# Optimization experiments

Hardware: AMD Instinct MI355X
Metric: run time of the kernel (lower is better)

## Reference

```python
import jax, jax.numpy as jnp
import numpy as np

FEATURE_SIZE = 100000
FIELD_SIZE = 39
EMBED_SIZE = 16
BATCH = 4096


def setup_inputs() -> dict:
    key = jax.random.key(0)
    k1, k2, k3, k4 = jax.random.split(key, 4)
    feature_idx = jax.random.randint(k1, (BATCH, FIELD_SIZE), 0, FEATURE_SIZE)
    feature_values = jax.random.uniform(k2, (BATCH, FIELD_SIZE), dtype=jnp.float32)
    feature_embeddings = jax.random.normal(
        k3, (FEATURE_SIZE, FIELD_SIZE, EMBED_SIZE), dtype=jnp.float32)
    weights_first_order = jax.random.normal(k4, (FEATURE_SIZE, 1), dtype=jnp.float32)
    fm_bias = jnp.zeros((1,), dtype=jnp.float32)
    return {
        "feature_idx": feature_idx,
        "feature_values": feature_values,
        "feature_embeddings": feature_embeddings,
        "weights_first_order": weights_first_order,
        "fm_bias": fm_bias,
    }


def reference(feature_idx, feature_values, feature_embeddings, weights_first_order, fm_bias):
    # First order: gather per-feature scalar weights -> [B, F]
    w1 = weights_first_order[feature_idx, 0]
    first_order = jnp.sum(feature_values * w1, axis=1, keepdims=True)  # [B,1]

    # Field-aware gather: E[b, i, f, :] = feature_embeddings[idx[b,i], f, :]
    E = feature_embeddings[feature_idx]  # [B, F, F, E]

    # S[b,i,j] = <v_{i,fj}, v_{j,fi}>  (dot over embedding dim)
    S = jnp.einsum('bije,bjie->bij', E, E)  # [B, F, F]

    vv = feature_values[:, :, None] * feature_values[:, None, :]  # [B, F, F]
    F = feature_idx.shape[1]
    upper = jnp.triu(jnp.ones((F, F), dtype=bool), k=1)  # i < j pairs
    second_order = jnp.sum(jnp.where(upper, S * vv, 0.0), axis=(1, 2))[:, None]  # [B,1]

    return second_order + first_order + fm_bias
```

## Files before the change

### kernel.cpp

```cpp
#include <hip/hip_runtime.h>
#include <hip/hip_fp16.h>

#define BATCH 4096
#define FIELD 39
#define EMBED 16
#define ROW_F4 (FIELD * EMBED / 4)
#define TOT_F4 (FIELD * ROW_F4)
#define NPAIRS (FIELD * (FIELD - 1))
#define NTASK2 (NPAIRS * 2)
#define BLOCK 1024
#define NWAVES (BLOCK / 64)
#define SITER ((TOT_F4 + BLOCK - 1) / BLOCK)
#define CITER ((NTASK2 + BLOCK - 1) / BLOCK)

__global__ __launch_bounds__(BLOCK, 8) void ffm_kernel(
    const int*   __restrict__ idx,
    const float* __restrict__ vals,
    const float* __restrict__ emb,
    const float* __restrict__ w1,
    const float* __restrict__ bias,
    float*       __restrict__ out)
{
    const int b   = blockIdx.x;
    const int tid = threadIdx.x;

    __shared__ __align__(16) __half s_emb[FIELD * FIELD * EMBED];
    __shared__ int    s_idx[FIELD];
    __shared__ float  s_val[FIELD];
    __shared__ float  s_red[NWAVES];

    if (tid < FIELD) {
        s_idx[tid] = idx[b * FIELD + tid];
        s_val[tid] = vals[b * FIELD + tid];
    }
    __syncthreads();

    const float4* emb4 = (const float4*)emb;
    float4 g[SITER];
    #pragma unroll
    for (int it = 0; it < SITER; ++it) {
        int t  = tid + it * BLOCK;
        int tc = t < TOT_F4 ? t : TOT_F4 - 1;
        int i  = tc / ROW_F4;
        int off = tc - i * ROW_F4;
        g[it] = emb4[s_idx[i] * ROW_F4 + off];
    }

    float acc = 0.0f;
    if (tid < FIELD) {
        acc = s_val[tid] * w1[s_idx[tid]];
    }

    __half2* s2 = (__half2*)s_emb;
    #pragma unroll
    for (int it = 0; it < SITER; ++it) {
        int t = tid + it * BLOCK;
        if (t < TOT_F4) {
            s2[t * 2]     = __floats2half2_rn(g[it].x, g[it].y);
            s2[t * 2 + 1] = __floats2half2_rn(g[it].z, g[it].w);
        }
    }
    __syncthreads();

    #pragma unroll
    for (int it = 0; it < CITER; ++it) {
        int t = tid + it * BLOCK;
        if (t < NTASK2) {
            int p = t >> 1;
            int h = t & 1;
            int i = p / (FIELD - 1);
            int r = p - i * (FIELD - 1);
            int j = r + (r >= i ? 1 : 0);
            float4 av = *(const float4*)&s_emb[(i * FIELD + j) * EMBED + h * 8];
            float4 cv = *(const float4*)&s_emb[(j * FIELD + i) * EMBED + h * 8];
            const __half2* ah = (const __half2*)&av;
            const __half2* ch = (const __half2*)&cv;
            float dot = 0.0f;
            #pragma unroll
            for (int k = 0; k < 4; ++k) {
                float2 a = __half22float2(ah[k]);
                float2 c = __half22float2(ch[k]);
                dot += a.x * c.x + a.y * c.y;
            }
            acc += dot * (0.5f * s_val[i] * s_val[j]);
        }
    }

    #pragma unroll
    for (int off = 32; off > 0; off >>= 1)
        acc += __shfl_down(acc, off, 64);

    const int wave = tid >> 6;
    const int lane = tid & 63;
    if (lane == 0) s_red[wave] = acc;
    __syncthreads();

    if (tid == 0) {
        float s = 0.0f;
        #pragma unroll
        for (int w = 0; w < NWAVES; ++w) s += s_red[w];
        out[b] = s + bias[0];
    }
}

extern "C" void kernel_launch(void* const* d_in, const int* in_sizes, int n_in,
                              void* d_out, int out_size, void* d_ws, size_t ws_size,
                              hipStream_t stream) {
    const int*   idx  = (const int*)d_in[0];
    const float* vals = (const float*)d_in[1];
    const float* emb  = (const float*)d_in[2];
    const float* w1   = (const float*)d_in[3];
    const float* bias = (const float*)d_in[4];
    float* out = (float*)d_out;

    ffm_kernel<<<BATCH, BLOCK, 0, stream>>>(idx, vals, emb, w1, bias, out);
}
```

Before: 344.6 us.

## Process multiple batch rows per block with prefetch of next row's embeddings

Switches from one block per batch row to a persistent grid of 512 blocks that each process 8 rows. While the current row's pairwise dot products run from shared memory, the next row's embedding gather is issued into registers, overlapping global loads with compute. Gather addresses are precomputed and packed once per block. In exchange there is less block-level parallelism, and holding the prefetched registers may raise register pressure.

```diff
diff --git a/kernel.cpp b/kernel.cpp
--- a/kernel.cpp
+++ b/kernel.cpp
@@ -2,16 +2,18 @@
 #include <hip/hip_fp16.h>
 
 #define BATCH 4096
-#define FIELD 39
-#define EMBED 16
-#define ROW_F4 (FIELD * EMBED / 4)
-#define TOT_F4 (FIELD * ROW_F4)
-#define NPAIRS (FIELD * (FIELD - 1))
+#define F 39
+#define E 16
+#define ROW_F4 (F * E / 4)
+#define TOT_F4 (F * ROW_F4)
+#define NPAIRS (F * (F - 1))
 #define NTASK2 (NPAIRS * 2)
 #define BLOCK 1024
 #define NWAVES (BLOCK / 64)
-#define SITER ((TOT_F4 + BLOCK - 1) / BLOCK)
-#define CITER ((NTASK2 + BLOCK - 1) / BLOCK)
+#define GRID 512
+#define ROWS (BATCH / GRID)
+#define SITER 6
+#define CITER 3
 
 __global__ __launch_bounds__(BLOCK, 8) void ffm_kernel(
     const int*   __restrict__ idx,
@@ -21,85 +23,104 @@
     const float* __restrict__ bias,
     float*       __restrict__ out)
 {
-    const int b   = blockIdx.x;
     const int tid = threadIdx.x;
+    const int b0  = blockIdx.x * ROWS;
 
-    __shared__ __align__(16) __half s_emb[FIELD * FIELD * EMBED];
-    __shared__ int    s_idx[FIELD];
-    __shared__ float  s_val[FIELD];
-    __shared__ float  s_red[NWAVES];
+    __shared__ __align__(16) __half s_emb[F * F * E];
+    __shared__ int   s_idx[ROWS][F];
+    __shared__ float s_val[ROWS][F];
+    __shared__ float s_red[NWAVES];
 
-    if (tid < FIELD) {
-        s_idx[tid] = idx[b * FIELD + tid];
-        s_val[tid] = vals[b * FIELD + tid];
+    if (tid < ROWS * F) {
+        ((int*)s_idx)[tid]   = idx[b0 * F + tid];
+        ((float*)s_val)[tid] = vals[b0 * F + tid];
     }
     __syncthreads();
 
-    const float4* emb4 = (const float4*)emb;
-    float4 g[SITER];
+    int cpk[SITER];
     #pragma unroll
-    for (int it = 0; it < SITER; ++it) {
-        int t  = tid + it * BLOCK;
+    for (int k = 0; k < SITER; ++k) {
+        int t  = tid + k * BLOCK;
         int tc = t < TOT_F4 ? t : TOT_F4 - 1;
-        int i  = tc / ROW_F4;
-        int off = tc - i * ROW_F4;
-        g[it] = emb4[s_idx[i] * ROW_F4 + off];
+        int ci = tc / ROW_F4;
+        cpk[k] = (ci << 16) | (tc - ci * ROW_F4);
     }
 
-    float acc = 0.0f;
-    if (tid < FIELD) {
-        acc = s_val[tid] * w1[s_idx[tid]];
-    }
+    const float4* emb4 = (const float4*)emb;
+    __half2* s2 = (__half2*)s_emb;
+    float4 g[SITER];
 
-    __half2* s2 = (__half2*)s_emb;
     #pragma unroll
-    for (int it = 0; it < SITER; ++it) {
-        int t = tid + it * BLOCK;
+    for (int k = 0; k < SITER; ++k)
+        g[k] = emb4[s_idx[0][cpk[k] >> 16] * ROW_F4 + (cpk[k] & 0xffff)];
+    #pragma unroll
+    for (int k = 0; k < SITER; ++k) {
+        int t = tid + k * BLOCK;
         if (t < TOT_F4) {
-            s2[t * 2]     = __floats2half2_rn(g[it].x, g[it].y);
-            s2[t * 2 + 1] = __floats2half2_rn(g[it].z, g[it].w);
+            s2[t * 2]     = __floats2half2_rn(g[k].x, g[k].y);
+            s2[t * 2 + 1] = __floats2half2_rn(g[k].z, g[k].w);
         }
     }
     __syncthreads();
 
-    #pragma unroll
-    for (int it = 0; it < CITER; ++it) {
-        int t = tid + it * BLOCK;
-        if (t < NTASK2) {
-            int p = t >> 1;
-            int h = t & 1;
-            int i = p / (FIELD - 1);
-            int r = p - i * (FIELD - 1);
-            int j = r + (r >= i ? 1 : 0);
-            float4 av = *(const float4*)&s_emb[(i * FIELD + j) * EMBED + h * 8];
-            float4 cv = *(const float4*)&s_emb[(j * FIELD + i) * EMBED + h * 8];
-            const __half2* ah = (const __half2*)&av;
-            const __half2* ch = (const __half2*)&cv;
-            float dot = 0.0f;
+    for (int r = 0; r < ROWS; ++r) {
+        if (r + 1 < ROWS) {
             #pragma unroll
-            for (int k = 0; k < 4; ++k) {
-                float2 a = __half22float2(ah[k]);
-                float2 c = __half22float2(ch[k]);
-                dot += a.x * c.x + a.y * c.y;
+            for (int k = 0; k < SITER; ++k)
+                g[k] = emb4[s_idx[r + 1][cpk[k] >> 16] * ROW_F4 + (cpk[k] & 0xffff)];
+        }
+
+        float acc = 0.0f;
+        if (tid < F) acc = s_val[r][tid] * w1[s_idx[r][tid]];
+
+        #pragma unroll
+        for (int it = 0; it < CITER; ++it) {
+            int t = tid + it * BLOCK;
+            if (t < NTASK2) {
+                int p = t >> 1;
+                int h = t & 1;
+                int i = p / (F - 1);
+                int q = p - i * (F - 1);
+                int j = q + (q >= i ? 1 : 0);
+                float4 av = *(const float4*)&s_emb[(i * F + j) * E + h * 8];
+                float4 cv = *(const float4*)&s_emb[(j * F + i) * E + h * 8];
+                const __half2* ah = (const __half2*)&av;
+                const __half2* ch = (const __half2*)&cv;
+                float dot = 0.0f;
+                #pragma unroll
+                for (int k = 0; k < 4; ++k) {
+                    float2 a = __half22float2(ah[k]);
+                    float2 c = __half22float2(ch[k]);
+                    dot += a.x * c.x + a.y * c.y;
+                }
+                acc += dot * (0.5f * s_val[r][i] * s_val[r][j]);
             }
-            acc += dot * (0.5f * s_val[i] * s_val[j]);
         }
-    }
 
-    #pragma unroll
-    for (int off = 32; off > 0; off >>= 1)
-        acc += __shfl_down(acc, off, 64);
+        #pragma unroll
+        for (int off = 32; off > 0; off >>= 1)
+            acc += __shfl_down(acc, off, 64);
+        if ((tid & 63) == 0) s_red[tid >> 6] = acc;
+        __syncthreads();
 
-    const int wave = tid >> 6;
-    const int lane = tid & 63;
-    if (lane == 0) s_red[wave] = acc;
-    __syncthreads();
+        if (tid == 0) {
+            float s = 0.0f;
+            #pragma unroll
+            for (int w = 0; w < NWAVES; ++w) s += s_red[w];
+            out[b0 + r] = s + bias[0];
+        }
 
-    if (tid == 0) {
-        float s = 0.0f;
-        #pragma unroll
-        for (int w = 0; w < NWAVES; ++w) s += s_red[w];
-        out[b] = s + bias[0];
+        if (r + 1 < ROWS) {
+            #pragma unroll
+            for (int k = 0; k < SITER; ++k) {
+                int t = tid + k * BLOCK;
+                if (t < TOT_F4) {
+                    s2[t * 2]     = __floats2half2_rn(g[k].x, g[k].y);
+                    s2[t * 2 + 1] = __floats2half2_rn(g[k].z, g[k].w);
+                }
+            }
+            __syncthreads();
+        }
     }
 }
 
@@ -113,5 +134,5 @@
     const float* bias = (const float*)d_in[4];
     float* out = (float*)d_out;
 
-    ffm_kernel<<<BATCH, BLOCK, 0, stream>>>(idx, vals, emb, w1, bias, out);
+    ffm_kernel<<<GRID, BLOCK, 0, stream>>>(idx, vals, emb, w1, bias, out);
 }
```

Measured after the change: 417.0 us. 1.21x slower.
